# Kernel tuning notes

Measured on AMD Instinct MI355X. Metric: run time of the kernel, lower is better.

## Reference

```python
import jax, jax.numpy as jnp
import numpy as np

T = 500        # num_target
R = 50         # num_resource
NS = 1000      # hard-coded sample count in the torch loop
F_STATE = 2    # raw state features; num_feature = F_STATE + T = 502
NOISE_F = 2
H1, H2 = 32, 16
NEG_SLOPE = 0.2


def _lrelu(x):
    return jnp.where(x >= 0, x, NEG_SLOPE * x)


def setup_inputs() -> dict:
    key = jax.random.key(0)
    ks = jax.random.split(key, 16)
    d = {}
    d["state"] = jax.random.normal(ks[0], (1, T, F_STATE), jnp.float32)
    d["def_cur_loc"] = jax.random.uniform(ks[1], (R, T), jnp.float32)
    d["feat_noise"] = jax.random.uniform(ks[2], (1, T, NOISE_F), jnp.float32)
    d["gumbel_u"] = jax.random.uniform(ks[3], (NS, R, T), jnp.float32, 1e-6, 1.0 - 1e-6)
    # learned / fixed parameters
    d["payoff"] = jax.random.normal(ks[4], (T, T), jnp.float32)
    # row-normalized adjacency surrogate
    a = jax.random.uniform(ks[5], (T, T), jnp.float32)
    d["norm_adj"] = a / jnp.sum(a, axis=1, keepdims=True)
    fin = F_STATE + T + NOISE_F  # 504 = num_feature + noise_feat
    d["gc1_w"] = jax.random.normal(ks[6], (fin, H1), jnp.float32) / np.sqrt(fin)
    d["gc1_b"] = jnp.zeros((H1,), jnp.float32)
    d["gc2_w"] = jax.random.normal(ks[7], (H1, H2), jnp.float32) / np.sqrt(H1)
    d["gc2_b"] = jnp.zeros((H2,), jnp.float32)
    d["bn_gamma"] = jnp.ones((T,), jnp.float32)
    d["bn_beta"] = jnp.zeros((T,), jnp.float32)
    d["actgen_w"] = jax.random.normal(ks[8], (H2 * T, T), jnp.float32) / np.sqrt(H2 * T)
    d["actgen_v"] = jax.random.normal(ks[9], (T, T), jnp.float32) / np.sqrt(T)
    return d


def reference(state, def_cur_loc, feat_noise, gumbel_u, payoff, norm_adj,
              gc1_w, gc1_b, gc2_w, gc2_b, bn_gamma, bn_beta,
              actgen_w, actgen_v):
    # x = cat(state, payoff, noise) -> (1, T, 504)
    x = jnp.concatenate([state, payoff[None], feat_noise], axis=2)

    def gcn(h, w, b):  # GraphConvolution: norm_adj @ (h @ w) + b
        return jnp.einsum('tu,buc->btc', norm_adj, h @ w) + b

    def bn(h):  # BatchNorm1d(T) in eval mode (running mean 0, var 1)
        return h * bn_gamma[None, :, None] + bn_beta[None, :, None]

    h = _lrelu(bn(gcn(x, gc1_w, gc1_b)))          # (1, T, 32); dropout is eval-mode identity
    h = _lrelu(bn(gcn(h, gc2_w, gc2_b)))          # (1, T, 16)
    xf = h.reshape(H2 * T)                        # x.view(-1, 16*T).squeeze()

    # act_gen: shared linear head + location projection -> per-resource logits (R, T)
    logits = xf @ actgen_w + def_cur_loc @ actgen_v

    # 1000 independent stochastic samples (the torch for-loop, fully batched):
    g = -jnp.log(-jnp.log(gumbel_u))              # (NS, R, T) gumbel noise
    act_estimates = jax.nn.softmax(logits[None] + g, axis=-1)  # (1000, R, T)
    # state_value head exists in the module but is not returned; omitted.
    return act_estimates
```

## Files before the change

### kernel.cpp

```cpp
#include <hip/hip_runtime.h>

#define T_ 500
#define R_ 50
#define NS_ 1000
#define H1_ 32
#define H2_ 16
#define NEG_ 0.2f

typedef float vf4 __attribute__((ext_vector_type(4)));

__device__ __forceinline__ float lrelu(float x) { return x >= 0.f ? x : NEG_ * x; }

__global__ __launch_bounds__(256) void k1_xw(const float* __restrict__ state,
                                             const float* __restrict__ payoff,
                                             const float* __restrict__ noise,
                                             const float* __restrict__ w,
                                             float* __restrict__ y1) {
    __shared__ float xs[504];
    __shared__ float red[8][H1_];
    int t = blockIdx.x, tid = threadIdx.x;
    for (int u = tid; u < T_; u += 256) xs[2 + u] = payoff[t * T_ + u];
    if (tid == 0) {
        xs[0] = state[t * 2];     xs[1] = state[t * 2 + 1];
        xs[502] = noise[t * 2];   xs[503] = noise[t * 2 + 1];
    }
    __syncthreads();
    int c = tid & 31, kg = tid >> 5;
    float acc = 0.f;
#pragma unroll 7
    for (int f = kg; f < 504; f += 8) acc += xs[f] * w[f * H1_ + c];
    red[kg][c] = acc;
    __syncthreads();
    if (tid < H1_) {
        float a = 0.f;
#pragma unroll
        for (int s = 0; s < 8; ++s) a += red[s][tid];
        y1[t * H1_ + tid] = a;
    }
}

__global__ __launch_bounds__(256) void k2_adj_fused(const float* __restrict__ adj,
                                                    const float* __restrict__ y1,
                                                    const float* __restrict__ b,
                                                    const float* __restrict__ gamma,
                                                    const float* __restrict__ beta,
                                                    const float* __restrict__ w2,
                                                    float* __restrict__ y2) {
    __shared__ float arow[T_];
    __shared__ float red[8][H1_];
    __shared__ float h1row[H1_];
    int t = blockIdx.x, tid = threadIdx.x;
    for (int u = tid; u < T_; u += 256) arow[u] = adj[t * T_ + u];
    __syncthreads();
    int c = tid & 31, kg = tid >> 5;
    float acc = 0.f;
#pragma unroll 4
    for (int u = kg; u < T_; u += 8) acc += arow[u] * y1[u * H1_ + c];
    red[kg][c] = acc;
    __syncthreads();
    if (tid < H1_) {
        float a = 0.f;
#pragma unroll
        for (int s = 0; s < 8; ++s) a += red[s][tid];
        h1row[tid] = lrelu((a + b[tid]) * gamma[t] + beta[t]);
    }
    __syncthreads();
    if (tid < H2_) {
        float a = 0.f;
#pragma unroll
        for (int cc = 0; cc < H1_; ++cc) a += h1row[cc] * w2[cc * H2_ + tid];
        y2[t * H2_ + tid] = a;
    }
}

__global__ __launch_bounds__(256) void k3_adj2_aw(const float* __restrict__ adj,
                                                  const float* __restrict__ y2,
                                                  const float* __restrict__ b2,
                                                  const float* __restrict__ gamma,
                                                  const float* __restrict__ beta,
                                                  const float* __restrict__ aw,
                                                  float* __restrict__ part1) {
    __shared__ float arow[T_];
    __shared__ float red[16][H2_];
    __shared__ float xfr[H2_];
    int t = blockIdx.x, tid = threadIdx.x;
    for (int u = tid; u < T_; u += 256) arow[u] = adj[t * T_ + u];
    __syncthreads();
    int c2 = tid & 15, kg = tid >> 4;
    float acc = 0.f;
#pragma unroll 4
    for (int u = kg; u < T_; u += 16) acc += arow[u] * y2[u * H2_ + c2];
    red[kg][c2] = acc;
    __syncthreads();
    if (tid < H2_) {
        float a = 0.f;
#pragma unroll
        for (int s = 0; s < 16; ++s) a += red[s][tid];
        xfr[tid] = lrelu((a + b2[tid]) * gamma[t] + beta[t]);
    }
    __syncthreads();
    float acc0 = 0.f, acc1 = 0.f;
#pragma unroll
    for (int c = 0; c < H2_; ++c) {
        float xv = xfr[c];
        const float* awr = aw + (t * H2_ + c) * T_;
        acc0 += xv * awr[tid];
        if (tid < T_ - 256) acc1 += xv * awr[256 + tid];
    }
    part1[t * T_ + tid] = acc0;
    if (tid < T_ - 256) part1[t * T_ + 256 + tid] = acc1;
}

__global__ __launch_bounds__(256) void k4_logits_part(const float* __restrict__ dloc,
                                                      const float* __restrict__ av,
                                                      const float* __restrict__ part1,
                                                      float* __restrict__ part2) {
    int r = blockIdx.x;
    int jb = blockIdx.y & 1, q = blockIdx.y >> 1;
    __shared__ float drow[125];
    int tid = threadIdx.x;
    int t0 = q * 125;
    if (tid < 125) drow[tid] = dloc[r * T_ + t0 + tid];
    __syncthreads();
    if (tid >= 250) return;
    int j = jb * 250 + tid;
    float acc = 0.f;
#pragma unroll 5
    for (int i = 0; i < 125; ++i) {
        int t = t0 + i;
        acc += drow[i] * av[t * T_ + j] + part1[t * T_ + j];
    }
    part2[q * (R_ * T_) + r * T_ + j] = acc;
}

__global__ __launch_bounds__(256) void k4_reduce_exp(const float* __restrict__ part2,
                                                     float* __restrict__ elog) {
    int gid = blockIdx.x * 256 + threadIdx.x;
    if (gid >= R_ * T_) return;
    float v = part2[gid] + part2[R_ * T_ + gid] +
              part2[2 * R_ * T_ + gid] + part2[3 * R_ * T_ + gid];
    elog[gid] = __expf(v);
}

__global__ __launch_bounds__(256) void k7_softmax(const float4* __restrict__ gu,
                                                  const float4* __restrict__ elog,
                                                  float* __restrict__ out) {
    int wave = threadIdx.x >> 6;
    int lane = threadIdx.x & 63;
    int row = blockIdx.x * 4 + wave;
    int r = row % R_;
    const float4* grow = gu + row * 125;
    const float4* erow = elog + r * 125;
    bool has1 = lane < 61;

    float4 g0 = grow[lane];
    float4 e0 = erow[lane];
    float4 g1, e1;
    if (has1) {
        g1 = grow[64 + lane];
        e1 = erow[64 + lane];
    }
    float p[8];
    p[0] = e0.x * __builtin_amdgcn_rcpf(-__log2f(g0.x));
    p[1] = e0.y * __builtin_amdgcn_rcpf(-__log2f(g0.y));
    p[2] = e0.z * __builtin_amdgcn_rcpf(-__log2f(g0.z));
    p[3] = e0.w * __builtin_amdgcn_rcpf(-__log2f(g0.w));
    if (has1) {
        p[4] = e1.x * __builtin_amdgcn_rcpf(-__log2f(g1.x));
        p[5] = e1.y * __builtin_amdgcn_rcpf(-__log2f(g1.y));
        p[6] = e1.z * __builtin_amdgcn_rcpf(-__log2f(g1.z));
        p[7] = e1.w * __builtin_amdgcn_rcpf(-__log2f(g1.w));
    } else {
        p[4] = p[5] = p[6] = p[7] = 0.f;
    }
    float s = ((p[0] + p[1]) + (p[2] + p[3])) + ((p[4] + p[5]) + (p[6] + p[7]));
#pragma unroll
    for (int off = 32; off > 0; off >>= 1) s += __shfl_xor(s, off);
    float inv = __builtin_amdgcn_rcpf(s);

    vf4* orow = (vf4*)(out + row * T_);
    vf4 o0 = {p[0] * inv, p[1] * inv, p[2] * inv, p[3] * inv};
    __builtin_nontemporal_store(o0, orow + lane);
    if (has1) {
        vf4 o1 = {p[4] * inv, p[5] * inv, p[6] * inv, p[7] * inv};
        __builtin_nontemporal_store(o1, orow + 64 + lane);
    }
}

extern "C" void kernel_launch(void* const* d_in, const int* in_sizes, int n_in,
                              void* d_out, int out_size, void* d_ws, size_t ws_size,
                              hipStream_t stream) {
    const float* state  = (const float*)d_in[0];
    const float* dloc   = (const float*)d_in[1];
    const float* noise  = (const float*)d_in[2];
    const float* gu     = (const float*)d_in[3];
    const float* payoff = (const float*)d_in[4];
    const float* adj    = (const float*)d_in[5];
    const float* g1w    = (const float*)d_in[6];
    const float* g1b    = (const float*)d_in[7];
    const float* g2w    = (const float*)d_in[8];
    const float* g2b    = (const float*)d_in[9];
    const float* gamma  = (const float*)d_in[10];
    const float* beta   = (const float*)d_in[11];
    const float* aw     = (const float*)d_in[12];
    const float* av     = (const float*)d_in[13];
    float* out = (float*)d_out;

    float* ws     = (float*)d_ws;
    float* y1     = ws;
    float* y2     = ws + 16000;
    float* part1  = ws + 24000;
    float* part2  = ws + 274000;
    float* elog   = ws + 374000;

    k1_xw<<<T_, 256, 0, stream>>>(state, payoff, noise, g1w, y1);
    k2_adj_fused<<<T_, 256, 0, stream>>>(adj, y1, g1b, gamma, beta, g2w, y2);
    k3_adj2_aw<<<T_, 256, 0, stream>>>(adj, y2, g2b, gamma, beta, aw, part1);
    k4_logits_part<<<dim3(R_, 8), 256, 0, stream>>>(dloc, av, part1, part2);
    k4_reduce_exp<<<(R_ * T_ + 255) / 256, 256, 0, stream>>>(part2, elog);
    k7_softmax<<<(NS_ * R_) / 4, 256, 0, stream>>>(
        (const float4*)gu, (const float4*)elog, (float*)out);
}
```

Baseline: 71.84 us.

## Make softmax kernel persistent with grid-stride rows and register prefetch

The final softmax kernel switches from one wave per row (12500 blocks) to a fixed grid of 2048 blocks. Each wave strides over rows and prefetches the next row's gumbel data into registers while computing the current row. The nontemporal output stores are replaced with plain float4 stores. The aim is to cut block launch overhead and hide global load latency, at the cost of less parallelism per row and possibly worse cache behaviour for the 100MB output stream.

```diff
diff --git a/kernel.cpp b/kernel.cpp
--- a/kernel.cpp
+++ b/kernel.cpp
@@ -6,8 +6,8 @@
 #define H1_ 32
 #define H2_ 16
 #define NEG_ 0.2f
-
-typedef float vf4 __attribute__((ext_vector_type(4)));
+#define NROWS_ (NS_ * R_)
+#define RSTRIDE_ 8192
 
 __device__ __forceinline__ float lrelu(float x) { return x >= 0.f ? x : NEG_ * x; }
 
@@ -144,46 +144,61 @@
 
 __global__ __launch_bounds__(256) void k7_softmax(const float4* __restrict__ gu,
                                                   const float4* __restrict__ elog,
-                                                  float* __restrict__ out) {
+                                                  float4* __restrict__ out) {
     int wave = threadIdx.x >> 6;
     int lane = threadIdx.x & 63;
-    int row = blockIdx.x * 4 + wave;
-    int r = row % R_;
-    const float4* grow = gu + row * 125;
-    const float4* erow = elog + r * 125;
+    int slot = blockIdx.x * 4 + wave;
     bool has1 = lane < 61;
 
-    float4 g0 = grow[lane];
-    float4 e0 = erow[lane];
-    float4 g1, e1;
-    if (has1) {
-        g1 = grow[64 + lane];
-        e1 = erow[64 + lane];
-    }
-    float p[8];
-    p[0] = e0.x * __builtin_amdgcn_rcpf(-__log2f(g0.x));
-    p[1] = e0.y * __builtin_amdgcn_rcpf(-__log2f(g0.y));
-    p[2] = e0.z * __builtin_amdgcn_rcpf(-__log2f(g0.z));
-    p[3] = e0.w * __builtin_amdgcn_rcpf(-__log2f(g0.w));
-    if (has1) {
-        p[4] = e1.x * __builtin_amdgcn_rcpf(-__log2f(g1.x));
-        p[5] = e1.y * __builtin_amdgcn_rcpf(-__log2f(g1.y));
-        p[6] = e1.z * __builtin_amdgcn_rcpf(-__log2f(g1.z));
-        p[7] = e1.w * __builtin_amdgcn_rcpf(-__log2f(g1.w));
-    } else {
-        p[4] = p[5] = p[6] = p[7] = 0.f;
-    }
-    float s = ((p[0] + p[1]) + (p[2] + p[3])) + ((p[4] + p[5]) + (p[6] + p[7]));
-#pragma unroll
-    for (int off = 32; off > 0; off >>= 1) s += __shfl_xor(s, off);
-    float inv = __builtin_amdgcn_rcpf(s);
-
-    vf4* orow = (vf4*)(out + row * T_);
-    vf4 o0 = {p[0] * inv, p[1] * inv, p[2] * inv, p[3] * inv};
-    __builtin_nontemporal_store(o0, orow + lane);
-    if (has1) {
-        vf4 o1 = {p[4] * inv, p[5] * inv, p[6] * inv, p[7] * inv};
-        __builtin_nontemporal_store(o1, orow + 64 + lane);
+    int row = slot;
+    float4 g0 = {1.f, 1.f, 1.f, 1.f}, g1 = {1.f, 1.f, 1.f, 1.f};
+    if (row < NROWS_) {
+        const float4* grow = gu + row * 125;
+        g0 = grow[lane];
+        if (has1) g1 = grow[64 + lane];
+    }
+    while (row < NROWS_) {
+        int nrow = row + RSTRIDE_;
+        float4 n0, n1;
+        if (nrow < NROWS_) {
+            const float4* ngrow = gu + nrow * 125;
+            n0 = ngrow[lane];
+            if (has1) n1 = ngrow[64 + lane];
+        }
+        int r = row % R_;
+        const float4* erow = elog + r * 125;
+        float4 e0 = erow[lane];
+        float4 e1;
+        if (has1) e1 = erow[64 + lane];
+
+        float p[8];
+        p[0] = e0.x * __builtin_amdgcn_rcpf(-__log2f(g0.x));
+        p[1] = e0.y * __builtin_amdgcn_rcpf(-__log2f(g0.y));
+        p[2] = e0.z * __builtin_amdgcn_rcpf(-__log2f(g0.z));
+        p[3] = e0.w * __builtin_amdgcn_rcpf(-__log2f(g0.w));
+        if (has1) {
+            p[4] = e1.x * __builtin_amdgcn_rcpf(-__log2f(g1.x));
+            p[5] = e1.y * __builtin_amdgcn_rcpf(-__log2f(g1.y));
+            p[6] = e1.z * __builtin_amdgcn_rcpf(-__log2f(g1.z));
+            p[7] = e1.w * __builtin_amdgcn_rcpf(-__log2f(g1.w));
+        } else {
+            p[4] = p[5] = p[6] = p[7] = 0.f;
+        }
+        float s = ((p[0] + p[1]) + (p[2] + p[3])) + ((p[4] + p[5]) + (p[6] + p[7]));
+#pragma unroll
+        for (int off = 32; off > 0; off >>= 1) s += __shfl_xor(s, off);
+        float inv = __builtin_amdgcn_rcpf(s);
+
+        float4* orow = out + row * 125;
+        float4 o0 = {p[0] * inv, p[1] * inv, p[2] * inv, p[3] * inv};
+        orow[lane] = o0;
+        if (has1) {
+            float4 o1 = {p[4] * inv, p[5] * inv, p[6] * inv, p[7] * inv};
+            orow[64 + lane] = o1;
+        }
+        row = nrow;
+        g0 = n0;
+        g1 = n1;
     }
 }
 
@@ -218,6 +233,6 @@
     k3_adj2_aw<<<T_, 256, 0, stream>>>(adj, y2, g2b, gamma, beta, aw, part1);
     k4_logits_part<<<dim3(R_, 8), 256, 0, stream>>>(dloc, av, part1, part2);
     k4_reduce_exp<<<(R_ * T_ + 255) / 256, 256, 0, stream>>>(part2, elog);
-    k7_softmax<<<(NS_ * R_) / 4, 256, 0, stream>>>(
-        (const float4*)gu, (const float4*)elog, (float*)out);
-}
+    k7_softmax<<<RSTRIDE_ / 4, 256, 0, stream>>>(
+        (const float4*)gu, (const float4*)elog, (float4*)out);
+}
```

New measurement: 72.55 us. No clear change (+1.0%).
